# Kernel tuning notes

Measured on AMD Instinct MI355X. Metric: run time of the kernel, lower is better.

Reference implementation:

```python
import jax, jax.numpy as jnp
import numpy as np

B, N, K, H, C, PE, EMB, OUT = 2, 2048, 16, 4, 8, 64, 1024, 2
P = C * (C + 1) // 2  # 36 unordered class pairs
RADIUS, NEG, EPS = 0.08, 0.2, 1e-5


def _ball_query(pos, radius, nsample):
    # pos [B,N,2] -> idx [B,N,nsample]; indices within radius, padded with first in-ball index
    sq = jnp.sum(pos * pos, -1)
    d = sq[:, :, None] + sq[:, None, :] - 2.0 * jnp.einsum('bnc,bmc->bnm', pos, pos)
    n = pos.shape[1]
    idx = jnp.broadcast_to(jnp.arange(n)[None, None, :], d.shape)
    idx = jnp.where(d > radius * radius, n, idx)
    idx = jnp.sort(idx, axis=-1)[:, :, :nsample]
    return jnp.where(idx == n, idx[:, :, :1], idx)


def _gather(feat, idx):
    # feat [B,F,N], idx [B,N,K] -> [B,F,N,K]
    return jnp.take_along_axis(feat[:, :, None, :], idx[:, None, :, :], axis=3)


def _pe(rel, dim):
    # sinusoidal encoding of relative coords rel [B,2,N,K] -> [B,dim,N,K]
    nf = dim // 4
    freqs = 10000.0 ** (-jnp.arange(nf, dtype=rel.dtype) / nf)
    ang = rel[:, :, None] * freqs[None, None, :, None, None]     # [B,2,nf,N,K]
    enc = jnp.concatenate([jnp.sin(ang), jnp.cos(ang)], axis=2)  # [B,2,2nf,N,K]
    b = enc.shape[0]
    return enc.reshape(b, dim, enc.shape[3], enc.shape[4])


def _conv(x, w, g, bvec):
    # 1x1 conv (no bias) + inference BN (running mean 0, var 1) + LeakyReLU
    y = jnp.einsum('oc,bc...->bo...', w, x) / jnp.sqrt(1.0 + EPS)
    sh = (1, -1) + (1,) * (y.ndim - 2)
    return jax.nn.leaky_relu(y * g.reshape(sh) + bvec.reshape(sh), NEG)


def _attn_layer(x, Ws, a_pairs, a_selfs, core, tgt):
    # PointpairAttentionLayer (per-class-pair coefficients), vmapped over heads.
    # x [B,F,N,K]; core [B,N] int; tgt [B,N,K] int
    s0 = jnp.minimum(tgt, core[:, :, None])
    s1 = jnp.maximum(tgt, core[:, :, None])
    pidx = s0 * C - (s0 * (s0 - 1)) // 2 + (s1 - s0)             # [B,N,K] pair index
    self_mask = (tgt[:, :, 0] < core)[:, :, None]                # slot-0 keeps a_self when pair-write happened earlier

    def head(W, a_pair, a_self):
        Wh = jnp.einsum('bfnk,fg->bnkg', x, W)                   # [B,N,K,F]
        a = a_pair[pidx]                                         # [B,N,K,F]
        slot0 = jnp.where(self_mask, a_self[core], a[:, :, 0])
        a = a.at[:, :, 0].set(slot0)
        e = jax.nn.leaky_relu(Wh * a, NEG)
        attn = jax.nn.softmax(e, axis=2)                         # over K neighbors
        return jax.nn.elu(attn * Wh)                             # [B,N,K,F]

    hs = jax.vmap(head)(Ws, a_pairs, a_selfs)                    # [H,B,N,K,F]
    b, n, k = x.shape[0], x.shape[2], x.shape[3]
    return jnp.transpose(hs, (1, 0, 4, 2, 3)).reshape(b, -1, n, k)


def _edge(feat, idx):
    # DGCNN edge features: concat(neighbor - center, center)
    tf = _gather(feat, idx)
    return jnp.concatenate([tf - feat[..., None],
                            jnp.broadcast_to(feat[..., None], tf.shape)], axis=1)


def _forward(pos, types, conv1_w, bn1_g, bn1_b, W1, ap1, as1,
             conv2_w, bn2_g, bn2_b, W2, ap2, as2,
             conv3_w, bn3_g, bn3_b, W3, ap3, as3,
             conv4_w, bn4_g, bn4_b, W4, ap4, as4,
             conv5_w, bn5_g, bn5_b, lin1_w, bn6_g, bn6_b,
             lin2_w, lin2_b, bn7_g, bn7_b, lin3_w, lin3_b):
    idx = _ball_query(pos, RADIUS, K)                            # [B,N,K]
    posT = jnp.transpose(pos, (0, 2, 1))                         # [B,2,N]
    rel = _gather(posT, idx) - posT[..., None]                   # [B,2,N,K]
    tgt = _gather(types[:, None, :], idx)[:, 0]                  # [B,N,K] neighbor classes

    x = _conv(_pe(rel, PE), conv1_w, bn1_g, bn1_b)               # [B,64,N,K]
    x1 = _attn_layer(x, W1, ap1, as1, types, tgt).sum(-1)        # [B,H*64,N]
    x = _conv(_edge(x1, idx), conv2_w, bn2_g, bn2_b)             # [B,64,N,K]
    x2 = _attn_layer(x, W2, ap2, as2, types, tgt).sum(-1)        # [B,H*64,N]
    x = _conv(_edge(x2, idx), conv3_w, bn3_g, bn3_b)             # [B,128,N,K]
    x3 = _attn_layer(x, W3, ap3, as3, types, tgt).sum(-1)        # [B,H*128,N]
    x = _conv(_edge(x3, idx), conv4_w, bn4_g, bn4_b)             # [B,256,N,K]
    x4 = _attn_layer(x, W4, ap4, as4, types, tgt).sum(-1)        # [B,H*256,N]

    xc = jnp.concatenate([x1, x2, x3, x4], axis=1)               # [B,H*512,N]
    x = _conv(xc, conv5_w, bn5_g, bn5_b)                         # [B,EMB,N]
    feat = jnp.concatenate([x.max(-1), x.mean(-1)], axis=-1)     # [B,2*EMB]

    def bn1d(y, g, bvec):
        return (y / jnp.sqrt(1.0 + EPS)) * g + bvec

    h = jax.nn.leaky_relu(bn1d(feat @ lin1_w.T, bn6_g, bn6_b), NEG)
    h = jax.nn.leaky_relu(bn1d(h @ lin2_w.T + lin2_b, bn7_g, bn7_b), NEG)
    return h @ lin3_w.T + lin3_b                                 # [B,OUT]


def setup_inputs() -> dict:
    key = jax.random.key(0)
    ks = iter(jax.random.split(key, 64))
    rn = lambda *s: jax.random.normal(next(ks), s, dtype=jnp.float32)
    d = {}
    d['pos'] = jax.random.uniform(next(ks), (B, N, 2), dtype=jnp.float32)
    d['types'] = jax.random.randint(next(ks), (B, N), 0, C, dtype=jnp.int32)

    def layer(f_in, f, tag):
        d['conv%d_w' % tag] = rn(f, f_in) * (1.0 / np.sqrt(f_in))
        d['bn%d_g' % tag] = jnp.ones((f,), jnp.float32)
        d['bn%d_b' % tag] = jnp.zeros((f,), jnp.float32)

    layer(PE, 64, 1)
    d['W1'] = rn(H, 64, 64) * 0.125; d['ap1'] = rn(H, P, 64) * 0.5; d['as1'] = rn(H, C, 64) * 0.5
    layer(2 * H * 64, 64, 2)
    d['W2'] = rn(H, 64, 64) * 0.125; d['ap2'] = rn(H, P, 64) * 0.5; d['as2'] = rn(H, C, 64) * 0.5
    layer(2 * H * 64, 128, 3)
    d['W3'] = rn(H, 128, 128) * 0.09; d['ap3'] = rn(H, P, 128) * 0.5; d['as3'] = rn(H, C, 128) * 0.5
    layer(2 * H * 128, 256, 4)
    d['W4'] = rn(H, 256, 256) * 0.0625; d['ap4'] = rn(H, P, 256) * 0.5; d['as4'] = rn(H, C, 256) * 0.5
    layer(H * 512, EMB, 5)
    d['lin1_w'] = rn(512, 2 * EMB) * 0.02
    d['bn6_g'] = jnp.ones((512,), jnp.float32); d['bn6_b'] = jnp.zeros((512,), jnp.float32)
    d['lin2_w'] = rn(256, 512) * 0.04; d['lin2_b'] = jnp.zeros((256,), jnp.float32)
    d['bn7_g'] = jnp.ones((256,), jnp.float32); d['bn7_b'] = jnp.zeros((256,), jnp.float32)
    d['lin3_w'] = rn(OUT, 256) * 0.06; d['lin3_b'] = jnp.zeros((OUT,), jnp.float32)
    return d


def reference(pos, types, conv1_w, bn1_g, bn1_b, W1, ap1, as1,
              conv2_w, bn2_g, bn2_b, W2, ap2, as2,
              conv3_w, bn3_g, bn3_b, W3, ap3, as3,
              conv4_w, bn4_g, bn4_b, W4, ap4, as4,
              conv5_w, bn5_g, bn5_b, lin1_w, bn6_g, bn6_b,
              lin2_w, lin2_b, bn7_g, bn7_b, lin3_w, lin3_b):
    return _forward(pos, types, conv1_w, bn1_g, bn1_b, W1, ap1, as1,
                    conv2_w, bn2_g, bn2_b, W2, ap2, as2,
                    conv3_w, bn3_g, bn3_b, W3, ap3, as3,
                    conv4_w, bn4_g, bn4_b, W4, ap4, as4,
                    conv5_w, bn5_g, bn5_b, lin1_w, bn6_g, bn6_b,
                    lin2_w, lin2_b, bn7_g, bn7_b, lin3_w, lin3_b)
```

## Files before the change

### kernel.cpp

```cpp
#include <hip/hip_runtime.h>
#include <math.h>

#define BB 2
#define NN 2048
#define KK 16
#define HH 4
#define CC 8
#define PP 36
#define NEGS 0.2f
#define INVS 0.9999950000374997f

typedef __attribute__((ext_vector_type(8))) short s16x8;
typedef __attribute__((ext_vector_type(8))) unsigned short u16x8;
typedef __attribute__((ext_vector_type(4))) float f32x4;

__device__ inline unsigned short bfh(float x) {
  unsigned u = __float_as_uint(x);
  return (unsigned short)((u + 0x7FFFu + ((u >> 16) & 1u)) >> 16);
}
__device__ inline float bff(unsigned short h) {
  return __uint_as_float(((unsigned)h) << 16);
}
__device__ inline f32x4 mfma16(s16x8 a, s16x8 b, f32x4 c) {
  return __builtin_amdgcn_mfma_f32_16x16x32_bf16(a, b, c, 0, 0, 0);
}

__global__ __launch_bounds__(256) void k_ballquery(const float* __restrict__ pos,
                                                   const int* __restrict__ types,
                                                   int* __restrict__ idxg,
                                                   int* __restrict__ acode,
                                                   float* __restrict__ rel) {
  __shared__ int s_buf[4][KK];
  const float r2 = (float)(0.08 * 0.08);
  int wslot = threadIdx.x >> 6;
  int lane = threadIdx.x & 63;
  int wg = blockIdx.x * 4 + wslot;
  int b = wg / NN, n = wg - b * NN;
  const float* pb = pos + (size_t)b * NN * 2;
  float px = pb[n * 2 + 0], py = pb[n * 2 + 1];
  float sqn = px * px + py * py;
  unsigned mask = 0u;
  int base = lane * 32;
  for (int j = 0; j < 32; ++j) {
    float qx = pb[(base + j) * 2 + 0], qy = pb[(base + j) * 2 + 1];
    float sqm = qx * qx + qy * qy;
    float d = sqn + sqm - 2.0f * (px * qx + py * qy);
    if (d <= r2) mask |= (1u << j);
  }
  int cnt = __popc(mask);
  int inc = cnt;
#pragma unroll
  for (int off = 1; off < 64; off <<= 1) {
    int v = __shfl_up(inc, off, 64);
    if (lane >= off) inc += v;
  }
  int total = __shfl(inc, 63, 64);
  int excl = inc - cnt;
  unsigned mm = mask;
  int p = excl;
  while (mm && p < KK) {
    int j = __ffs(mm) - 1;
    mm &= mm - 1u;
    s_buf[wslot][p] = base + j;
    ++p;
  }
  __syncthreads();
  int tc = total < KK ? total : KK;
  if (lane < KK) {
    int m0 = s_buf[wslot][0];
    int mk = (lane < tc) ? s_buf[wslot][lane] : m0;
    idxg[wg * KK + lane] = mk;
    int core = types[b * NN + n];
    int tg = types[b * NN + mk];
    int s0 = tg < core ? tg : core;
    int s1 = tg < core ? core : tg;
    int code = s0 * CC - (s0 * (s0 - 1)) / 2 + (s1 - s0);
    if (lane == 0 && tg < core) code = PP + core;
    acode[wg * KK + lane] = code;
    rel[(wg * KK + lane) * 2 + 0] = pb[mk * 2 + 0] - px;
    rel[(wg * KK + lane) * 2 + 1] = pb[mk * 2 + 1] - py;
  }
}

struct PackDesc {
  const float* src;
  unsigned short* dh;
  unsigned short* dl;
  int KB, NT, srcld, Cdiff, mode, sstride, dstride, nrep, bpr;
};
struct PackArgs {
  PackDesc d[20];
};
__global__ __launch_bounds__(256) void k_megapack(PackArgs pa) {
  PackDesc D = pa.d[blockIdx.y];
  int rep = blockIdx.x / D.bpr;
  if (rep >= D.nrep) return;
  int f = (blockIdx.x - rep * D.bpr) * 256 + threadIdx.x;
  int total = D.KB * D.NT * 64;
  if (f >= total) return;
  const float* src = D.src + (size_t)rep * D.sstride;
  unsigned short* dh = D.dh + (size_t)rep * D.dstride;
  if (D.mode == 3) {
    if (f * 8 >= D.Cdiff) return;
    float* dd = (float*)dh;
    size_t o = (size_t)f * 8;
#pragma unroll
    for (int i = 0; i < 8; ++i) dd[o + i] = src[o + i];
    return;
  }
  unsigned short* dl = D.dl + (size_t)rep * D.dstride;
  int l = f & 63;
  int t2 = f >> 6;
  int n = (t2 / D.KB) * 16 + (l & 15);
  int k0 = (t2 % D.KB) * 32 + ((l >> 4) * 8);
  size_t o = (size_t)t2 * 512 + (size_t)l * 8;
#pragma unroll
  for (int i = 0; i < 8; ++i) {
    int k = k0 + i;
    float v;
    if (D.mode == 0) {
      v = src[(size_t)k * D.srcld + n];
    } else if (D.mode == 1) {
      v = src[(size_t)n * D.srcld + k];
    } else {
      v = src[(size_t)n * D.srcld + k + D.Cdiff] - src[(size_t)n * D.srcld + k];
    }
    unsigned short hi = bfh(v);
    dh[o + i] = hi;
    dl[o + i] = bfh(v - bff(hi));
  }
}

template <int KBW, int NTB>
__global__ __launch_bounds__(512, 4) void k_pregemm(
    const unsigned short* __restrict__ xh, int xoff,
    const unsigned short* __restrict__ wph, const unsigned short* __restrict__ wpl,
    const float* __restrict__ scale, const float* __restrict__ bias,
    float* __restrict__ ouv, int cout) {
  constexpr int NCH = KBW / 2;
  constexpr int JT = NTB / 2;
  const int ld = 2 * cout;
  __shared__ alignas(16) char s_mem[32768];
  int tid = threadIdx.x;
  int lane = tid & 63;
  int w = tid >> 6;
  int lg = lane >> 4;
  int ln = lane & 15;
  int bm = blockIdx.x;
  int ntoff = blockIdx.y * NTB;
  int wm = w >> 1, wn = w & 1;
  f32x4 acc[2][JT];
#pragma unroll
  for (int m = 0; m < 2; ++m)
#pragma unroll
    for (int j = 0; j < JT; ++j) acc[m][j] = (f32x4){0.f, 0.f, 0.f, 0.f};

  int srowg = bm * 128 + w * 16 + ln;
  const unsigned short* gH = xh + (size_t)srowg * 2048 + xoff + lg * 8;
  int wbyA = ((w * 2 + 0) * 64 + lane) * 16;
  int wbyB = ((w * 2 + 1) * 64 + lane) * 16;
  u16x8 h0, h1;
  auto load2 = [&](int ch) {
    h0 = *(const u16x8*)(gH + ch * 64);
    h1 = *(const u16x8*)(gH + ch * 64 + 32);
  };
  load2(0);
  *(u16x8*)(s_mem + wbyA) = h0;
  *(u16x8*)(s_mem + wbyB) = h1;
  __syncthreads();
  int p = 0;
  for (int ch = 0; ch < NCH; ++ch) {
    if (ch + 1 < NCH) load2(ch + 1);
#pragma unroll
    for (int ks = 0; ks < 2; ++ks) {
      s16x8 ah[2];
#pragma unroll
      for (int m = 0; m < 2; ++m) {
        int by = p * 16384 + (((wm * 2 + m) * 2 + ks) * 64 + lane) * 16;
        ah[m] = *(const s16x8*)(s_mem + by);
      }
      int kb = ch * 2 + ks;
      __builtin_amdgcn_s_setprio(1);
#pragma unroll
      for (int j = 0; j < JT; ++j) {
        size_t fo = ((size_t)(ntoff + wn * JT + j) * KBW + kb) * 64 + lane;
        s16x8 bh = ((const s16x8*)wph)[fo];
        s16x8 bl = ((const s16x8*)wpl)[fo];
#pragma unroll
        for (int m = 0; m < 2; ++m) {
          acc[m][j] = mfma16(ah[m], bh, acc[m][j]);
          acc[m][j] = mfma16(ah[m], bl, acc[m][j]);
        }
      }
      __builtin_amdgcn_s_setprio(0);
    }
    if (ch + 1 < NCH) {
      int d = (p ^ 1) * 16384;
      *(u16x8*)(s_mem + d + wbyA) = h0;
      *(u16x8*)(s_mem + d + wbyB) = h1;
      p ^= 1;
    }
    __syncthreads();
  }
#pragma unroll
  for (int j = 0; j < JT; ++j) {
    int g = (ntoff + wn * JT + j) * 16 + ln;
    int gm = g >= cout ? g - cout : g;
    float sc = scale[gm] * INVS;
    float bs = (g >= cout) ? bias[gm] : 0.f;
#pragma unroll
    for (int m = 0; m < 2; ++m) {
#pragma unroll
      for (int reg = 0; reg < 4; ++reg) {
        int row = bm * 128 + wm * 32 + m * 16 + lg * 4 + reg;
        ouv[(size_t)row * ld + g] = acc[m][j][reg] * sc + bs;
      }
    }
  }
}

template <int FOUT>
__device__ __forceinline__ void attn_phase(
    const char* s_mem, const int* s_code, unsigned short* xh, int pgbase,
    int w, int lane, const unsigned short* __restrict__ attnh,
    const unsigned short* __restrict__ attnl, const float* __restrict__ coef,
    int ooff) {
  constexpr int KBA = FOUT / 32;
  constexpr int NT = FOUT / 16;
  constexpr int NTW_A = NT / 2;
  constexpr int JW = (NTW_A > 2) ? 2 : NTW_A;
  constexpr int NPASS = NTW_A / JW;
  int lg = lane >> 4;
  int ln = lane & 15;
  int h = w >> 1, nh = w & 1;
  const s16x8* wph = (const s16x8*)(attnh + (size_t)h * FOUT * FOUT);
  const s16x8* wpl = (const s16x8*)(attnl + (size_t)h * FOUT * FOUT);
  const float* hb = coef + (size_t)h * 44 * FOUT + ln;
#pragma unroll 1
  for (int pass = 0; pass < NPASS; ++pass) {
    float ac[4][JW][4];
#pragma unroll
    for (int m = 0; m < 4; ++m)
#pragma unroll
      for (int reg = 0; reg < 4; ++reg) {
        int off = s_code[m * 16 + lg * 4 + reg] * FOUT;
#pragma unroll
        for (int j = 0; j < JW; ++j) {
          int nt = nh * NTW_A + pass * JW + j;
          ac[m][j][reg] = hb[off + nt * 16];
        }
      }
    f32x4 aacc[4][JW];
#pragma unroll
    for (int m = 0; m < 4; ++m)
#pragma unroll
      for (int j = 0; j < JW; ++j) aacc[m][j] = (f32x4){0.f, 0.f, 0.f, 0.f};
#pragma unroll 2
    for (int kb = 0; kb < KBA; ++kb) {
      s16x8 ah[4];
#pragma unroll
      for (int m = 0; m < 4; ++m) {
        int by = ((m * KBA + kb) * 64 + lane) * 16;
        ah[m] = *(const s16x8*)(s_mem + by);
      }
      __builtin_amdgcn_s_setprio(1);
#pragma unroll
      for (int j = 0; j < JW; ++j) {
        int nt = nh * NTW_A + pass * JW + j;
        size_t fo = ((size_t)nt * KBA + kb) * 64 + lane;
        s16x8 bh = wph[fo];
        s16x8 bl = wpl[fo];
#pragma unroll
        for (int m = 0; m < 4; ++m) {
          aacc[m][j] = mfma16(ah[m], bh, aacc[m][j]);
          aacc[m][j] = mfma16(ah[m], bl, aacc[m][j]);
        }
      }
      __builtin_amdgcn_s_setprio(0);
    }
#pragma unroll
    for (int m = 0; m < 4; ++m) {
      int pg = pgbase + m;
#pragma unroll
      for (int j = 0; j < JW; ++j) {
        int nt = nh * NTW_A + pass * JW + j;
        int g = nt * 16 + ln;
        float e[4];
        float ssum = 0.f;
#pragma unroll
        for (int reg = 0; reg < 4; ++reg) {
          float ev = aacc[m][j][reg] * ac[m][j][reg];
          ev = (ev >= 0.f) ? ev : NEGS * ev;
          float pe = __expf(ev);
          e[reg] = pe;
          ssum += pe;
        }
        ssum += __shfl_xor(ssum, 16, 64);
        ssum += __shfl_xor(ssum, 32, 64);
        float inv = 1.f / ssum;
        float o = 0.f;
#pragma unroll
        for (int reg = 0; reg < 4; ++reg) {
          float u = e[reg] * inv * aacc[m][j][reg];
          o += (u > 0.f) ? u : (__expf(u) - 1.f);
        }
        o += __shfl_xor(o, 16, 64);
        o += __shfl_xor(o, 32, 64);
        if (lane < 16) {
          xh[(size_t)pg * 2048 + ooff + h * FOUT + g] = bfh(o);
        }
      }
    }
  }
}

template <int FOUT>
__global__ __launch_bounds__(512, 4) void k_attn(
    unsigned short* xh, const float* __restrict__ uv,
    const int* __restrict__ idx, const int* __restrict__ acode,
    const unsigned short* __restrict__ attnh, const unsigned short* __restrict__ attnl,
    const float* __restrict__ coef, int ooff) {
  constexpr int KBA = FOUT / 32;
  constexpr int YPLANE = 64 * FOUT * 2;
  constexpr int FPW = (4 * KBA) / 8;
  constexpr int C2 = 2 * FOUT;

  __shared__ alignas(16) char s_mem[YPLANE];
  __shared__ int s_gsrc[64];
  __shared__ int s_code[64];

  int tid = threadIdx.x;
  int lane = tid & 63;
  int w = tid >> 6;
  int lg = lane >> 4;
  int ln = lane & 15;
  int pgbase = blockIdx.x * 4;

  if (tid < 64) {
    int pg = pgbase + (tid >> 4);
    int b = pg >> 11;
    s_gsrc[tid] = b * 2048 + idx[pg * KK + (tid & 15)];
    s_code[tid] = acode[pg * KK + (tid & 15)];
  }
  __syncthreads();

#pragma unroll
  for (int r = 0; r < FPW; ++r) {
    int f = w * FPW + r;
    int mt = f / KBA, kb = f % KBA;
    int row = mt * 16 + ln;
    int col = kb * 32 + lg * 8;
    const float* up = uv + (size_t)s_gsrc[row] * C2 + col;
    const float* cp = uv + (size_t)(pgbase + mt) * C2 + FOUT + col;
    float4 u0 = *(const float4*)up;
    float4 u1 = *(const float4*)(up + 4);
    float4 v0 = *(const float4*)cp;
    float4 v1 = *(const float4*)(cp + 4);
    float uu[8] = {u0.x, u0.y, u0.z, u0.w, u1.x, u1.y, u1.z, u1.w};
    float vv[8] = {v0.x, v0.y, v0.z, v0.w, v1.x, v1.y, v1.z, v1.w};
    unsigned short oh[8];
#pragma unroll
    for (int i = 0; i < 8; ++i) {
      float t = uu[i] + vv[i];
      t = (t >= 0.f) ? t : NEGS * t;
      oh[i] = bfh(t);
    }
    *(u16x8*)(s_mem + (f * 64 + lane) * 16) = *(u16x8*)oh;
  }
  __syncthreads();

  attn_phase<FOUT>(s_mem, s_code, xh, pgbase, w, lane, attnh, attnl, coef, ooff);
}

__global__ __launch_bounds__(512, 4) void k_layer1(
    unsigned short* xh, const float* __restrict__ rel, const int* __restrict__ idx,
    const int* __restrict__ acode,
    const unsigned short* __restrict__ convh, const unsigned short* __restrict__ convl,
    const unsigned short* __restrict__ attnh, const unsigned short* __restrict__ attnl,
    const float* __restrict__ bng, const float* __restrict__ bnb,
    const float* __restrict__ coef, int ooff) {
  constexpr int FOUT = 64;
  constexpr int KB = 2;
  constexpr int KBA = 2;
  constexpr int YPLANE = 64 * FOUT * 2;

  __shared__ alignas(16) char s_mem[YPLANE];
  __shared__ int s_gsrc[64];
  __shared__ int s_code[64];

  int tid = threadIdx.x;
  int lane = tid & 63;
  int w = tid >> 6;
  int lg = lane >> 4;
  int ln = lane & 15;
  int pgbase = blockIdx.x * 4;

  if (tid < 64) {
    int pg = pgbase + (tid >> 4);
    int b = pg >> 11;
    s_gsrc[tid] = b * 2048 + idx[pg * KK + (tid & 15)];
    s_code[tid] = acode[pg * KK + (tid & 15)];
  }
  __syncthreads();

  {
    int smt = w >> 1, skb = w & 1;
    float rc = rel[((size_t)(pgbase + smt) * KK + ln) * 2 + skb];
    unsigned short hb[8];
#pragma unroll
    for (int i = 0; i < 8; ++i) {
      int j = lg * 8 + i;
      int fidx = j & 15;
      float freq = exp2f(-(float)fidx * 0.8304820237218406f);
      float ang = rc * freq;
      float v = (j < 16) ? __sinf(ang) : __cosf(ang);
      hb[i] = bfh(v);
    }
    *(u16x8*)(s_mem + ((w * 64 + lane) * 16)) = *(u16x8*)hb;
  }
  __syncthreads();

  int wr = w >> 2, wc = w & 3;
  f32x4 cacc[2];
  cacc[0] = (f32x4){0.f, 0.f, 0.f, 0.f};
  cacc[1] = (f32x4){0.f, 0.f, 0.f, 0.f};
#pragma unroll
  for (int ks = 0; ks < 2; ++ks) {
    s16x8 ah[2];
#pragma unroll
    for (int m = 0; m < 2; ++m) {
      int by = (((wr * 2 + m) * 2 + ks) * 64 + lane) * 16;
      ah[m] = *(const s16x8*)(s_mem + by);
    }
    __builtin_amdgcn_s_setprio(1);
    size_t fo = ((size_t)wc * KB + ks) * 64 + lane;
    s16x8 bh = ((const s16x8*)convh)[fo];
    s16x8 bl = ((const s16x8*)convl)[fo];
#pragma unroll
    for (int m = 0; m < 2; ++m) {
      cacc[m] = mfma16(ah[m], bh, cacc[m]);
      cacc[m] = mfma16(ah[m], bl, cacc[m]);
    }
    __builtin_amdgcn_s_setprio(0);
  }
  __syncthreads();

  {
    int g = wc * 16 + ln;
    float sc = bng[g] * INVS;
    float bs = bnb[g];
    int gpart = ((g >> 5) * 64 + ((g >> 3) & 3) * 16) * 16 + (g & 7) * 2;
#pragma unroll
    for (int m = 0; m < 2; ++m) {
#pragma unroll
      for (int reg = 0; reg < 4; ++reg) {
        int r = wr * 32 + m * 16 + lg * 4 + reg;
        float v = cacc[m][reg] * sc + bs;
        v = (v >= 0.f) ? v : NEGS * v;
        int by = (r >> 4) * (KBA * 1024) + gpart + (r & 15) * 16;
        *(unsigned short*)(s_mem + by) = bfh(v);
      }
    }
  }
  __syncthreads();

  attn_phase<64>(s_mem, s_code, xh, pgbase, w, lane, attnh, attnl, coef, ooff);
}

__global__ __launch_bounds__(512, 4) void k_gemm5_m(const unsigned short* __restrict__ xh,
                                                    const unsigned short* __restrict__ bph,
                                                    const unsigned short* __restrict__ bpl,
                                                    const float* __restrict__ g5,
                                                    const float* __restrict__ b5,
                                                    float* __restrict__ pmax,
                                                    float* __restrict__ psum) {
  __shared__ alignas(16) char s_mem[32768];
  int tid = threadIdx.x;
  int lane = tid & 63;
  int w = tid >> 6;
  int lg = lane >> 4;
  int ln = lane & 15;
  int bm = blockIdx.x, bn = blockIdx.y;
  int wm = w >> 2, wn = w & 3;
  f32x4 acc[4][2];
#pragma unroll
  for (int m = 0; m < 4; ++m)
#pragma unroll
    for (int j = 0; j < 2; ++j) acc[m][j] = (f32x4){0.f, 0.f, 0.f, 0.f};

  int srowg = bm * 128 + w * 16 + ln;
  const unsigned short* gH = xh + (size_t)srowg * 2048 + lg * 8;
  int wbyA = ((w * 2 + 0) * 64 + lane) * 16;
  int wbyB = ((w * 2 + 1) * 64 + lane) * 16;
  u16x8 h0, h1;
  auto load2 = [&](int ch) {
    h0 = *(const u16x8*)(gH + ch * 64);
    h1 = *(const u16x8*)(gH + ch * 64 + 32);
  };
  load2(0);
  *(u16x8*)(s_mem + wbyA) = h0;
  *(u16x8*)(s_mem + wbyB) = h1;
  __syncthreads();
  int p = 0;
  for (int ch = 0; ch < 32; ++ch) {
    if (ch + 1 < 32) load2(ch + 1);
#pragma unroll
    for (int ks = 0; ks < 2; ++ks) {
      s16x8 ah[4];
#pragma unroll
      for (int m = 0; m < 4; ++m) {
        int by = p * 16384 + (((wm * 4 + m) * 2 + ks) * 64 + lane) * 16;
        ah[m] = *(const s16x8*)(s_mem + by);
      }
      int kb = ch * 2 + ks;
      __builtin_amdgcn_s_setprio(1);
#pragma unroll
      for (int j = 0; j < 2; ++j) {
        size_t fo = ((size_t)(bn * 8 + wn * 2 + j) * 64 + kb) * 64 + lane;
        s16x8 bh = ((const s16x8*)bph)[fo];
        s16x8 bl = ((const s16x8*)bpl)[fo];
#pragma unroll
        for (int m = 0; m < 4; ++m) {
          acc[m][j] = mfma16(ah[m], bh, acc[m][j]);
          acc[m][j] = mfma16(ah[m], bl, acc[m][j]);
        }
      }
      __builtin_amdgcn_s_setprio(0);
    }
    if (ch + 1 < 32) {
      int d = (p ^ 1) * 16384;
      *(u16x8*)(s_mem + d + wbyA) = h0;
      *(u16x8*)(s_mem + d + wbyB) = h1;
      p ^= 1;
    }
    __syncthreads();
  }

  float cmax[2], csum[2];
#pragma unroll
  for (int j = 0; j < 2; ++j) {
    int g = bn * 128 + wn * 32 + j * 16 + ln;
    float sc = g5[g] * INVS;
    float bs = b5[g];
    float mx = -3.0e38f, sm = 0.f;
#pragma unroll
    for (int m = 0; m < 4; ++m)
#pragma unroll
      for (int reg = 0; reg < 4; ++reg) {
        float v = acc[m][j][reg] * sc + bs;
        v = (v >= 0.f) ? v : NEGS * v;
        mx = fmaxf(mx, v);
        sm += v;
      }
    mx = fmaxf(mx, __shfl_xor(mx, 16, 64));
    mx = fmaxf(mx, __shfl_xor(mx, 32, 64));
    sm += __shfl_xor(sm, 16, 64);
    sm += __shfl_xor(sm, 32, 64);
    cmax[j] = mx;
    csum[j] = sm;
  }
  float* s_f = (float*)s_mem;
  if (lg == 0) {
#pragma unroll
    for (int j = 0; j < 2; ++j) {
      int col = wn * 32 + j * 16 + ln;
      s_f[(wm * 128 + col) * 2 + 0] = cmax[j];
      s_f[(wm * 128 + col) * 2 + 1] = csum[j];
    }
  }
  __syncthreads();
  if (tid < 128) {
    float mx = fmaxf(s_f[tid * 2], s_f[(128 + tid) * 2]);
    float sm = s_f[tid * 2 + 1] + s_f[(128 + tid) * 2 + 1];
    pmax[(size_t)bm * 1024 + bn * 128 + tid] = mx;
    psum[(size_t)bm * 1024 + bn * 128 + tid] = sm;
  }
}

__global__ __launch_bounds__(256) void k_feat(const float* __restrict__ pmax,
                                              const float* __restrict__ psum,
                                              float* __restrict__ feat) {
  int t = blockIdx.x * 256 + threadIdx.x;
  if (t >= BB * 1024) return;
  int b = t >> 10, o = t & 1023;
  float mx = -3.0e38f, sm = 0.f;
  for (int i = 0; i < 16; ++i) {
    mx = fmaxf(mx, pmax[(size_t)(b * 16 + i) * 1024 + o]);
    sm += psum[(size_t)(b * 16 + i) * 1024 + o];
  }
  feat[b * 2048 + o] = mx;
  feat[b * 2048 + 1024 + o] = sm * (1.0f / NN);
}

template <bool HASB, bool DOBN, bool ACT>
__global__ __launch_bounds__(256) void k_head(const float* __restrict__ X,
                                              const float* __restrict__ Wm,
                                              const float* __restrict__ bias,
                                              const float* __restrict__ g,
                                              const float* __restrict__ bb,
                                              float* __restrict__ Y, int IN, int ON) {
  int gt = blockIdx.x * 256 + threadIdx.x;
  int w = gt >> 6, lane = gt & 63;
  if (w >= BB * ON) return;
  int b = w / ON, o = w - b * ON;
  const float* x = X + (size_t)b * IN;
  const float* wr = Wm + (size_t)o * IN;
  float s = 0.f;
  for (int c = lane; c < IN; c += 64) s += x[c] * wr[c];
#pragma unroll
  for (int off = 32; off > 0; off >>= 1) s += __shfl_down(s, off, 64);
  if (lane == 0) {
    if (HASB) s += bias[o];
    if (DOBN) s = s * INVS * g[o] + bb[o];
    if (ACT) s = (s >= 0.f) ? s : NEGS * s;
    Y[(size_t)b * ON + o] = s;
  }
}

extern "C" void kernel_launch(void* const* d_in, const int* in_sizes, int n_in,
                              void* d_out, int out_size, void* d_ws, size_t ws_size,
                              hipStream_t stream) {
  const float* pos = (const float*)d_in[0];
  const int* types = (const int*)d_in[1];
  const float* conv1_w = (const float*)d_in[2];
  const float* bn1_g = (const float*)d_in[3];
  const float* bn1_b = (const float*)d_in[4];
  const float* W1 = (const float*)d_in[5];
  const float* ap1 = (const float*)d_in[6];
  const float* as1 = (const float*)d_in[7];
  const float* conv2_w = (const float*)d_in[8];
  const float* bn2_g = (const float*)d_in[9];
  const float* bn2_b = (const float*)d_in[10];
  const float* W2 = (const float*)d_in[11];
  const float* ap2 = (const float*)d_in[12];
  const float* as2 = (const float*)d_in[13];
  const float* conv3_w = (const float*)d_in[14];
  const float* bn3_g = (const float*)d_in[15];
  const float* bn3_b = (const float*)d_in[16];
  const float* W3 = (const float*)d_in[17];
  const float* ap3 = (const float*)d_in[18];
  const float* as3 = (const float*)d_in[19];
  const float* conv4_w = (const float*)d_in[20];
  const float* bn4_g = (const float*)d_in[21];
  const float* bn4_b = (const float*)d_in[22];
  const float* W4 = (const float*)d_in[23];
  const float* ap4 = (const float*)d_in[24];
  const float* as4 = (const float*)d_in[25];
  const float* conv5_w = (const float*)d_in[26];
  const float* bn5_g = (const float*)d_in[27];
  const float* bn5_b = (const float*)d_in[28];
  const float* lin1_w = (const float*)d_in[29];
  const float* bn6_g = (const float*)d_in[30];
  const float* bn6_b = (const float*)d_in[31];
  const float* lin2_w = (const float*)d_in[32];
  const float* lin2_b = (const float*)d_in[33];
  const float* bn7_g = (const float*)d_in[34];
  const float* bn7_b = (const float*)d_in[35];
  const float* lin3_w = (const float*)d_in[36];
  const float* lin3_b = (const float*)d_in[37];
  (void)in_sizes; (void)n_in; (void)out_size; (void)ws_size;

  float* ws = (float*)d_ws;
  size_t off = 0;
  auto take = [&](size_t nf) {
    float* p = ws + off;
    off += (nf + 63) & ~(size_t)63;
    return p;
  };
  auto takeu = [&](size_t nu) { return (unsigned short*)take((nu + 1) / 2); };

  int* idx = (int*)take(BB * NN * KK);
  int* acode = (int*)take(BB * NN * KK);
  float* rel = take((size_t)BB * NN * KK * 2);
  unsigned short* xh = takeu((size_t)BB * NN * 2048);
  float* uv = take((size_t)4096 * 512);
  float* pmax = take(32 * 1024);
  float* psum = take(32 * 1024);
  float* feat = take(BB * 2048);
  float* h1 = take(BB * 512);
  float* h2 = take(BB * 256);
  unsigned short* c1h = takeu(64 * 64);
  unsigned short* c1l = takeu(64 * 64);
  unsigned short* uvw2h = takeu(256 * 128);
  unsigned short* uvw2l = takeu(256 * 128);
  unsigned short* uvw3h = takeu(256 * 256);
  unsigned short* uvw3l = takeu(256 * 256);
  unsigned short* uvw4h = takeu(512 * 512);
  unsigned short* uvw4l = takeu(512 * 512);
  unsigned short* a1h = takeu(4 * 64 * 64);
  unsigned short* a1l = takeu(4 * 64 * 64);
  unsigned short* a2h = takeu(4 * 64 * 64);
  unsigned short* a2l = takeu(4 * 64 * 64);
  unsigned short* a3h = takeu(4 * 128 * 128);
  unsigned short* a3l = takeu(4 * 128 * 128);
  unsigned short* a4h = takeu(4 * 256 * 256);
  unsigned short* a4l = takeu(4 * 256 * 256);
  unsigned short* g5h = takeu((size_t)2048 * 1024);
  unsigned short* g5l = takeu((size_t)2048 * 1024);
  float* coef1 = take(4 * 44 * 64);
  float* coef2 = take(4 * 44 * 64);
  float* coef3 = take(4 * 44 * 128);
  float* coef4 = take(4 * 44 * 256);

  dim3 blk(256);
  dim3 blk5(512);

  PackArgs pa;
  pa.d[0] = {conv1_w, c1h, c1l, 2, 4, 64, 0, 1, 0, 0, 1, 2};
  pa.d[1] = {conv2_w, uvw2h, uvw2l, 8, 4, 512, 0, 1, 0, 0, 1, 8};
  pa.d[2] = {conv2_w, uvw2h + 16384, uvw2l + 16384, 8, 4, 512, 256, 2, 0, 0, 1, 8};
  pa.d[3] = {conv3_w, uvw3h, uvw3l, 8, 8, 512, 0, 1, 0, 0, 1, 16};
  pa.d[4] = {conv3_w, uvw3h + 32768, uvw3l + 32768, 8, 8, 512, 256, 2, 0, 0, 1, 16};
  pa.d[5] = {conv4_w, uvw4h, uvw4l, 16, 16, 1024, 0, 1, 0, 0, 1, 64};
  pa.d[6] = {conv4_w, uvw4h + 131072, uvw4l + 131072, 16, 16, 1024, 512, 2, 0, 0, 1, 64};
  pa.d[7] = {W1, a1h, a1l, 2, 4, 64, 0, 0, 4096, 4096, 4, 2};
  pa.d[8] = {W2, a2h, a2l, 2, 4, 64, 0, 0, 4096, 4096, 4, 2};
  pa.d[9] = {W3, a3h, a3l, 4, 8, 128, 0, 0, 16384, 16384, 4, 8};
  pa.d[10] = {W4, a4h, a4l, 8, 16, 256, 0, 0, 65536, 65536, 4, 32};
  pa.d[11] = {conv5_w, g5h, g5l, 64, 64, 2048, 0, 1, 0, 0, 1, 1024};
  pa.d[12] = {ap1, (unsigned short*)coef1, nullptr, 5, 1, 0, 2304, 3, 2304, 5632, 4, 2};
  pa.d[13] = {as1, (unsigned short*)(coef1 + 2304), nullptr, 1, 1, 0, 512, 3, 512, 5632, 4, 1};
  pa.d[14] = {ap2, (unsigned short*)coef2, nullptr, 5, 1, 0, 2304, 3, 2304, 5632, 4, 2};
  pa.d[15] = {as2, (unsigned short*)(coef2 + 2304), nullptr, 1, 1, 0, 512, 3, 512, 5632, 4, 1};
  pa.d[16] = {ap3, (unsigned short*)coef3, nullptr, 9, 1, 0, 4608, 3, 4608, 11264, 4, 3};
  pa.d[17] = {as3, (unsigned short*)(coef3 + 4608), nullptr, 2, 1, 0, 1024, 3, 1024, 11264, 4, 1};
  pa.d[18] = {ap4, (unsigned short*)coef4, nullptr, 18, 1, 0, 9216, 3, 9216, 22528, 4, 5};
  pa.d[19] = {as4, (unsigned short*)(coef4 + 9216), nullptr, 4, 1, 0, 2048, 3, 2048, 22528, 4, 1};
  k_megapack<<<dim3(1024, 20), blk, 0, stream>>>(pa);

  k_ballquery<<<dim3(BB * NN / 4), blk, 0, stream>>>(pos, types, idx, acode, rel);

  k_layer1<<<dim3(BB * NN / 4), blk5, 0, stream>>>(
      xh, rel, idx, acode, c1h, c1l, a1h, a1l, bn1_g, bn1_b, coef1, 0);

  k_pregemm<8, 4><<<dim3(32, 2), blk5, 0, stream>>>(
      xh, 0, uvw2h, uvw2l, bn2_g, bn2_b, uv, 64);
  k_attn<64><<<dim3(BB * NN / 4), blk5, 0, stream>>>(
      xh, uv, idx, acode, a2h, a2l, coef2, 256);

  k_pregemm<8, 8><<<dim3(32, 2), blk5, 0, stream>>>(
      xh, 256, uvw3h, uvw3l, bn3_g, bn3_b, uv, 128);
  k_attn<128><<<dim3(BB * NN / 4), blk5, 0, stream>>>(
      xh, uv, idx, acode, a3h, a3l, coef3, 512);

  k_pregemm<16, 8><<<dim3(32, 4), blk5, 0, stream>>>(
      xh, 512, uvw4h, uvw4l, bn4_g, bn4_b, uv, 256);
  k_attn<256><<<dim3(BB * NN / 4), blk5, 0, stream>>>(
      xh, uv, idx, acode, a4h, a4l, coef4, 1024);

  k_gemm5_m<<<dim3(32, 8), blk5, 0, stream>>>(xh, g5h, g5l, bn5_g, bn5_b, pmax, psum);
  k_feat<<<dim3(8), blk, 0, stream>>>(pmax, psum, feat);
  k_head<false, true, true><<<dim3(BB * 512 * 64 / 256), blk, 0, stream>>>(
      feat, lin1_w, nullptr, bn6_g, bn6_b, h1, 2048, 512);
  k_head<true, true, true><<<dim3(BB * 256 * 64 / 256), blk, 0, stream>>>(
      h1, lin2_w, lin2_b, bn7_g, bn7_b, h2, 512, 256);
  k_head<true, false, false><<<dim3(1), blk, 0, stream>>>(
      h2, lin3_w, lin3_b, nullptr, nullptr, (float*)d_out, 256, 2);
}
```

Measured before the change: 381.8 us.

## Double attention block points to eight and retile gemm5 to 256-row blocks

Attention kernels now process 8 points per block instead of 4, so each loaded weight fragment feeds 8 M-tiles; JW drops to 1 to keep register use bounded. The final gemm5 kernel is retiled to 256 rows by 64 columns per block, with a 64KB LDS double buffer and two blocks per CU, which halves the partial max/sum count reduced in k_feat. The aim is more reuse of the B-operand weight loads per MFMA, at the cost of fewer blocks, lower occupancy and higher register and LDS pressure.

New measurement: 349.5 us (median of 2 runs). 1.09x faster.

```diff
diff --git a/kernel.cpp b/kernel.cpp
--- a/kernel.cpp
+++ b/kernel.cpp
@@ -219,7 +219,7 @@
   }
 }
 
-template <int FOUT>
+template <int FOUT, int MT>
 __device__ __forceinline__ void attn_phase(
     const char* s_mem, const int* s_code, unsigned short* xh, int pgbase,
     int w, int lane, const unsigned short* __restrict__ attnh,
@@ -228,7 +228,7 @@
   constexpr int KBA = FOUT / 32;
   constexpr int NT = FOUT / 16;
   constexpr int NTW_A = NT / 2;
-  constexpr int JW = (NTW_A > 2) ? 2 : NTW_A;
+  constexpr int JW = (MT == 8) ? 1 : ((NTW_A > 2) ? 2 : NTW_A);
   constexpr int NPASS = NTW_A / JW;
   int lg = lane >> 4;
   int ln = lane & 15;
@@ -238,9 +238,9 @@
   const float* hb = coef + (size_t)h * 44 * FOUT + ln;
 #pragma unroll 1
   for (int pass = 0; pass < NPASS; ++pass) {
-    float ac[4][JW][4];
-#pragma unroll
-    for (int m = 0; m < 4; ++m)
+    float ac[MT][JW][4];
+#pragma unroll
+    for (int m = 0; m < MT; ++m)
 #pragma unroll
       for (int reg = 0; reg < 4; ++reg) {
         int off = s_code[m * 16 + lg * 4 + reg] * FOUT;
@@ -250,16 +250,16 @@
           ac[m][j][reg] = hb[off + nt * 16];
         }
       }
-    f32x4 aacc[4][JW];
-#pragma unroll
-    for (int m = 0; m < 4; ++m)
+    f32x4 aacc[MT][JW];
+#pragma unroll
+    for (int m = 0; m < MT; ++m)
 #pragma unroll
       for (int j = 0; j < JW; ++j) aacc[m][j] = (f32x4){0.f, 0.f, 0.f, 0.f};
 #pragma unroll 2
     for (int kb = 0; kb < KBA; ++kb) {
-      s16x8 ah[4];
-#pragma unroll
-      for (int m = 0; m < 4; ++m) {
+      s16x8 ah[MT];
+#pragma unroll
+      for (int m = 0; m < MT; ++m) {
         int by = ((m * KBA + kb) * 64 + lane) * 16;
         ah[m] = *(const s16x8*)(s_mem + by);
       }
@@ -271,7 +271,7 @@
         s16x8 bh = wph[fo];
         s16x8 bl = wpl[fo];
 #pragma unroll
-        for (int m = 0; m < 4; ++m) {
+        for (int m = 0; m < MT; ++m) {
           aacc[m][j] = mfma16(ah[m], bh, aacc[m][j]);
           aacc[m][j] = mfma16(ah[m], bl, aacc[m][j]);
         }
@@ -279,7 +279,7 @@
       __builtin_amdgcn_s_setprio(0);
     }
 #pragma unroll
-    for (int m = 0; m < 4; ++m) {
+    for (int m = 0; m < MT; ++m) {
       int pg = pgbase + m;
 #pragma unroll
       for (int j = 0; j < JW; ++j) {
@@ -320,23 +320,24 @@
     const int* __restrict__ idx, const int* __restrict__ acode,
     const unsigned short* __restrict__ attnh, const unsigned short* __restrict__ attnl,
     const float* __restrict__ coef, int ooff) {
+  constexpr int MT = 8;
   constexpr int KBA = FOUT / 32;
-  constexpr int YPLANE = 64 * FOUT * 2;
-  constexpr int FPW = (4 * KBA) / 8;
+  constexpr int YPLANE = MT * 16 * FOUT * 2;
+  constexpr int FPW = (MT * KBA) / 8;
   constexpr int C2 = 2 * FOUT;
 
   __shared__ alignas(16) char s_mem[YPLANE];
-  __shared__ int s_gsrc[64];
-  __shared__ int s_code[64];
+  __shared__ int s_gsrc[MT * 16];
+  __shared__ int s_code[MT * 16];
 
   int tid = threadIdx.x;
   int lane = tid & 63;
   int w = tid >> 6;
   int lg = lane >> 4;
   int ln = lane & 15;
-  int pgbase = blockIdx.x * 4;
-
-  if (tid < 64) {
+  int pgbase = blockIdx.x * MT;
+
+  if (tid < MT * 16) {
     int pg = pgbase + (tid >> 4);
     int b = pg >> 11;
     s_gsrc[tid] = b * 2048 + idx[pg * KK + (tid & 15)];
@@ -369,7 +370,7 @@
   }
   __syncthreads();
 
-  attn_phase<FOUT>(s_mem, s_code, xh, pgbase, w, lane, attnh, attnl, coef, ooff);
+  attn_phase<FOUT, MT>(s_mem, s_code, xh, pgbase, w, lane, attnh, attnl, coef, ooff);
 }
 
 __global__ __launch_bounds__(512, 4) void k_layer1(
@@ -464,17 +465,17 @@
   }
   __syncthreads();
 
-  attn_phase<64>(s_mem, s_code, xh, pgbase, w, lane, attnh, attnl, coef, ooff);
-}
-
-__global__ __launch_bounds__(512, 4) void k_gemm5_m(const unsigned short* __restrict__ xh,
+  attn_phase<64, 4>(s_mem, s_code, xh, pgbase, w, lane, attnh, attnl, coef, ooff);
+}
+
+__global__ __launch_bounds__(512, 2) void k_gemm5_m(const unsigned short* __restrict__ xh,
                                                     const unsigned short* __restrict__ bph,
                                                     const unsigned short* __restrict__ bpl,
                                                     const float* __restrict__ g5,
                                                     const float* __restrict__ b5,
                                                     float* __restrict__ pmax,
                                                     float* __restrict__ psum) {
-  __shared__ alignas(16) char s_mem[32768];
+  __shared__ alignas(16) char s_mem[65536];
   int tid = threadIdx.x;
   int lane = tid & 63;
   int w = tid >> 6;
@@ -482,72 +483,79 @@
   int ln = lane & 15;
   int bm = blockIdx.x, bn = blockIdx.y;
   int wm = w >> 2, wn = w & 3;
-  f32x4 acc[4][2];
-#pragma unroll
-  for (int m = 0; m < 4; ++m)
-#pragma unroll
-    for (int j = 0; j < 2; ++j) acc[m][j] = (f32x4){0.f, 0.f, 0.f, 0.f};
-
-  int srowg = bm * 128 + w * 16 + ln;
-  const unsigned short* gH = xh + (size_t)srowg * 2048 + lg * 8;
-  int wbyA = ((w * 2 + 0) * 64 + lane) * 16;
-  int wbyB = ((w * 2 + 1) * 64 + lane) * 16;
-  u16x8 h0, h1;
-  auto load2 = [&](int ch) {
+  f32x4 acc[8];
+#pragma unroll
+  for (int m = 0; m < 8; ++m) acc[m] = (f32x4){0.f, 0.f, 0.f, 0.f};
+
+  int sr = w * 16 + ln;
+  const unsigned short* gH = xh + (size_t)(bm * 256 + sr) * 2048 + lg * 8;
+  const unsigned short* gH2 = gH + (size_t)128 * 2048;
+  int fm = sr >> 4;
+  int fl = lg * 16 + (sr & 15);
+  int wbyA = ((fm * 2 + 0) * 64 + fl) * 16;
+  int wbyB = ((fm * 2 + 1) * 64 + fl) * 16;
+  int wbyC = (((fm + 8) * 2 + 0) * 64 + fl) * 16;
+  int wbyD = (((fm + 8) * 2 + 1) * 64 + fl) * 16;
+  u16x8 h0, h1, h2, h3;
+  auto load4 = [&](int ch) {
     h0 = *(const u16x8*)(gH + ch * 64);
     h1 = *(const u16x8*)(gH + ch * 64 + 32);
+    h2 = *(const u16x8*)(gH2 + ch * 64);
+    h3 = *(const u16x8*)(gH2 + ch * 64 + 32);
   };
-  load2(0);
+  load4(0);
   *(u16x8*)(s_mem + wbyA) = h0;
   *(u16x8*)(s_mem + wbyB) = h1;
+  *(u16x8*)(s_mem + wbyC) = h2;
+  *(u16x8*)(s_mem + wbyD) = h3;
   __syncthreads();
   int p = 0;
   for (int ch = 0; ch < 32; ++ch) {
-    if (ch + 1 < 32) load2(ch + 1);
+    if (ch + 1 < 32) load4(ch + 1);
 #pragma unroll
     for (int ks = 0; ks < 2; ++ks) {
-      s16x8 ah[4];
-#pragma unroll
-      for (int m = 0; m < 4; ++m) {
-        int by = p * 16384 + (((wm * 4 + m) * 2 + ks) * 64 + lane) * 16;
+      s16x8 ah[8];
+#pragma unroll
+      for (int m = 0; m < 8; ++m) {
+        int by = p * 32768 + (((wm * 8 + m) * 2 + ks) * 64 + lane) * 16;
         ah[m] = *(const s16x8*)(s_mem + by);
       }
       int kb = ch * 2 + ks;
       __builtin_amdgcn_s_setprio(1);
-#pragma unroll
-      for (int j = 0; j < 2; ++j) {
-        size_t fo = ((size_t)(bn * 8 + wn * 2 + j) * 64 + kb) * 64 + lane;
+      {
+        size_t fo = ((size_t)(bn * 4 + wn) * 64 + kb) * 64 + lane;
         s16x8 bh = ((const s16x8*)bph)[fo];
         s16x8 bl = ((const s16x8*)bpl)[fo];
 #pragma unroll
-        for (int m = 0; m < 4; ++m) {
-          acc[m][j] = mfma16(ah[m], bh, acc[m][j]);
-          acc[m][j] = mfma16(ah[m], bl, acc[m][j]);
+        for (int m = 0; m < 8; ++m) {
+          acc[m] = mfma16(ah[m], bh, acc[m]);
+          acc[m] = mfma16(ah[m], bl, acc[m]);
         }
       }
       __builtin_amdgcn_s_setprio(0);
     }
     if (ch + 1 < 32) {
-      int d = (p ^ 1) * 16384;
+      int d = (p ^ 1) * 32768;
       *(u16x8*)(s_mem + d + wbyA) = h0;
       *(u16x8*)(s_mem + d + wbyB) = h1;
+      *(u16x8*)(s_mem + d + wbyC) = h2;
+      *(u16x8*)(s_mem + d + wbyD) = h3;
       p ^= 1;
     }
     __syncthreads();
   }
 
-  float cmax[2], csum[2];
-#pragma unroll
-  for (int j = 0; j < 2; ++j) {
-    int g = bn * 128 + wn * 32 + j * 16 + ln;
+  float cmax, csum;
+  {
+    int g = bn * 64 + wn * 16 + ln;
     float sc = g5[g] * INVS;
     float bs = b5[g];
     float mx = -3.0e38f, sm = 0.f;
 #pragma unroll
-    for (int m = 0; m < 4; ++m)
+    for (int m = 0; m < 8; ++m)
 #pragma unroll
       for (int reg = 0; reg < 4; ++reg) {
-        float v = acc[m][j][reg] * sc + bs;
+        float v = acc[m][reg] * sc + bs;
         v = (v >= 0.f) ? v : NEGS * v;
         mx = fmaxf(mx, v);
         sm += v;
@@ -556,24 +564,21 @@
     mx = fmaxf(mx, __shfl_xor(mx, 32, 64));
     sm += __shfl_xor(sm, 16, 64);
     sm += __shfl_xor(sm, 32, 64);
-    cmax[j] = mx;
-    csum[j] = sm;
+    cmax = mx;
+    csum = sm;
   }
   float* s_f = (float*)s_mem;
   if (lg == 0) {
-#pragma unroll
-    for (int j = 0; j < 2; ++j) {
-      int col = wn * 32 + j * 16 + ln;
-      s_f[(wm * 128 + col) * 2 + 0] = cmax[j];
-      s_f[(wm * 128 + col) * 2 + 1] = csum[j];
-    }
-  }
-  __syncthreads();
-  if (tid < 128) {
-    float mx = fmaxf(s_f[tid * 2], s_f[(128 + tid) * 2]);
-    float sm = s_f[tid * 2 + 1] + s_f[(128 + tid) * 2 + 1];
-    pmax[(size_t)bm * 1024 + bn * 128 + tid] = mx;
-    psum[(size_t)bm * 1024 + bn * 128 + tid] = sm;
+    int col = wn * 16 + ln;
+    s_f[(wm * 64 + col) * 2 + 0] = cmax;
+    s_f[(wm * 64 + col) * 2 + 1] = csum;
+  }
+  __syncthreads();
+  if (tid < 64) {
+    float mx = fmaxf(s_f[tid * 2], s_f[(64 + tid) * 2]);
+    float sm = s_f[tid * 2 + 1] + s_f[(64 + tid) * 2 + 1];
+    pmax[(size_t)bm * 1024 + bn * 64 + tid] = mx;
+    psum[(size_t)bm * 1024 + bn * 64 + tid] = sm;
   }
 }
 
@@ -584,9 +589,9 @@
   if (t >= BB * 1024) return;
   int b = t >> 10, o = t & 1023;
   float mx = -3.0e38f, sm = 0.f;
-  for (int i = 0; i < 16; ++i) {
-    mx = fmaxf(mx, pmax[(size_t)(b * 16 + i) * 1024 + o]);
-    sm += psum[(size_t)(b * 16 + i) * 1024 + o];
+  for (int i = 0; i < 8; ++i) {
+    mx = fmaxf(mx, pmax[(size_t)(b * 8 + i) * 1024 + o]);
+    sm += psum[(size_t)(b * 8 + i) * 1024 + o];
   }
   feat[b * 2048 + o] = mx;
   feat[b * 2048 + 1024 + o] = sm * (1.0f / NN);
@@ -674,8 +679,8 @@
   float* rel = take((size_t)BB * NN * KK * 2);
   unsigned short* xh = takeu((size_t)BB * NN * 2048);
   float* uv = take((size_t)4096 * 512);
-  float* pmax = take(32 * 1024);
-  float* psum = take(32 * 1024);
+  float* pmax = take(16 * 1024);
+  float* psum = take(16 * 1024);
   float* feat = take(BB * 2048);
   float* h1 = take(BB * 512);
   float* h2 = take(BB * 256);
@@ -735,20 +740,20 @@
 
   k_pregemm<8, 4><<<dim3(32, 2), blk5, 0, stream>>>(
       xh, 0, uvw2h, uvw2l, bn2_g, bn2_b, uv, 64);
-  k_attn<64><<<dim3(BB * NN / 4), blk5, 0, stream>>>(
+  k_attn<64><<<dim3(BB * NN / 8), blk5, 0, stream>>>(
       xh, uv, idx, acode, a2h, a2l, coef2, 256);
 
   k_pregemm<8, 8><<<dim3(32, 2), blk5, 0, stream>>>(
       xh, 256, uvw3h, uvw3l, bn3_g, bn3_b, uv, 128);
-  k_attn<128><<<dim3(BB * NN / 4), blk5, 0, stream>>>(
+  k_attn<128><<<dim3(BB * NN / 8), blk5, 0, stream>>>(
       xh, uv, idx, acode, a3h, a3l, coef3, 512);
 
   k_pregemm<16, 8><<<dim3(32, 4), blk5, 0, stream>>>(
       xh, 512, uvw4h, uvw4l, bn4_g, bn4_b, uv, 256);
-  k_attn<256><<<dim3(BB * NN / 4), blk5, 0, stream>>>(
+  k_attn<256><<<dim3(BB * NN / 8), blk5, 0, stream>>>(
       xh, uv, idx, acode, a4h, a4l, coef4, 1024);
 
-  k_gemm5_m<<<dim3(32, 8), blk5, 0, stream>>>(xh, g5h, g5l, bn5_g, bn5_b, pmax, psum);
+  k_gemm5_m<<<dim3(16, 16), blk5, 0, stream>>>(xh, g5h, g5l, bn5_g, bn5_b, pmax, psum);
   k_feat<<<dim3(8), blk, 0, stream>>>(pmax, psum, feat);
   k_head<false, true, true><<<dim3(BB * 512 * 64 / 256), blk, 0, stream>>>(
       feat, lin1_w, nullptr, bn6_g, bn6_b, h1, 2048, 512);
```
